# Kernel tuning notes

Hardware: AMD Instinct MI355X
Metric: run time of the kernel (lower is better)

## Reference

```python
import jax, jax.numpy as jnp
import numpy as np

N_NODES = 100000
N_EDGES = 1600000
D = 128

def setup_inputs() -> dict:
    key = jax.random.key(0)
    ks = jax.random.split(key, 6)
    x = jax.random.normal(ks[0], (N_NODES, D), dtype=jnp.float32)
    edge_src = jax.random.randint(ks[1], (N_EDGES,), 0, N_NODES, dtype=jnp.int32)
    edge_dst = jax.random.randint(ks[2], (N_EDGES,), 0, N_NODES, dtype=jnp.int32)
    # Glorot-ish scaling for 128x128 linears
    scale = 1.0 / np.sqrt(D)
    W1 = jax.random.normal(ks[3], (D, D), dtype=jnp.float32) * scale
    b1 = jnp.zeros((D,), dtype=jnp.float32)
    W2 = jax.random.normal(ks[4], (D, D), dtype=jnp.float32) * scale
    b2 = jnp.zeros((D,), dtype=jnp.float32)
    return {"x": x, "edge_src": edge_src, "edge_dst": edge_dst,
            "W1": W1, "b1": b1, "W2": W2, "b2": b2}

def reference(x, edge_src, edge_dst, W1, b1, W2, b2):
    # g.set_data('.hidden', data); g.apply(pre_mod): Linear + ReLU per node
    h = jax.nn.relu(x @ W1 + b1)                      # [N, D]
    # g.push(func=sum): each node's hidden becomes the sum of its
    # in-neighbors' hidden features (gather by src, scatter-add by dst).
    msgs = h[edge_src]                                # [E, D] irregular gather
    agg = jax.ops.segment_sum(msgs, edge_dst, num_segments=N_NODES)  # [N, D]
    # g.apply(post_mod): Linear per node; g.pop_data returns result
    out = agg @ W2 + b2                               # [N, D]
    return out
```

## Files before the change

kernel.cpp:

```cpp
#include <hip/hip_runtime.h>

#define D 128
#define NPB 256
#define NBMAX 512
#define BKCAP 8192
#define CHUNK 8192
#define OVF_CAP 8192

typedef __attribute__((ext_vector_type(8))) short short8x;
typedef __attribute__((ext_vector_type(4))) float f32x4;

__device__ inline unsigned int f2bf(float f) {
    unsigned int u = __builtin_bit_cast(unsigned int, f);
    return (u + 0x7fffu + ((u >> 16) & 1u)) >> 16;
}
__device__ inline float bflo(unsigned int v) {
    return __builtin_bit_cast(float, v << 16);
}
__device__ inline float bfhi(unsigned int v) {
    return __builtin_bit_cast(float, v & 0xffff0000u);
}
__device__ inline unsigned int pack2(float lo, float hi) {
    return f2bf(lo) | (f2bf(hi) << 16);
}

__global__ __launch_bounds__(256) void pack_w(
    const float* __restrict__ W1, const float* __restrict__ W2,
    uint4* __restrict__ pack, int* __restrict__ zero_area, int nz)
{
    if (blockIdx.x == 16) {
        for (int i = threadIdx.x; i < nz; i += 256) zero_area[i] = 0;
        return;
    }
    int e = blockIdx.x * 256 + threadIdx.x;
    const float* W = (e & 2048) ? W2 : W1;
    int f = (e >> 6) & 31, l = e & 63;
    int kt = f >> 3, nt = f & 7;
    int k0 = kt * 32 + (l >> 4) * 8;
    int col = nt * 16 + (l & 15);
    unsigned int v[8];
#pragma unroll
    for (int j = 0; j < 8; ++j) v[j] = f2bf(W[(size_t)(k0 + j) * D + col]);
    uint4 o;
    o.x = v[0] | (v[1] << 16);
    o.y = v[2] | (v[3] << 16);
    o.z = v[4] | (v[5] << 16);
    o.w = v[6] | (v[7] << 16);
    pack[e] = o;
}

__global__ __launch_bounds__(256) void build_gemm(
    const int* __restrict__ esrc, const int* __restrict__ edst,
    int* __restrict__ gfill, unsigned* __restrict__ pairs,
    int* __restrict__ ovf_cnt, int2* __restrict__ ovf_list, int E, int NB,
    int nscatter,
    const float* __restrict__ xin, const uint4* __restrict__ wpack,
    const float* __restrict__ b1, uint4* __restrict__ zout4, int n_rows)
{
    __shared__ __align__(16) char smem[65536];
    const int t = threadIdx.x;

    if (blockIdx.x < nscatter) {
        int* lcnt  = (int*)smem;
        int* lbase = lcnt + NBMAX;
        for (int b = t; b < NB; b += 256) lcnt[b] = 0;
        __syncthreads();
        int cb = blockIdx.x * CHUNK;
        int ce = min(E, cb + CHUNK);
        for (int i = cb + t; i < ce; i += 256)
            atomicAdd(&lcnt[edst[i] >> 8], 1);
        __syncthreads();
        for (int b = t; b < NB; b += 256) {
            int c = lcnt[b];
            lbase[b] = c ? atomicAdd(&gfill[b], c) : 0;
            lcnt[b] = 0;
        }
        __syncthreads();
        for (int i = cb + t; i < ce; i += 256) {
            int d = edst[i];
            int s = esrc[i];
            int b = d >> 8;
            int pos = lbase[b] + atomicAdd(&lcnt[b], 1);
            if (pos < BKCAP) {
                pairs[(size_t)b * BKCAP + pos] = ((unsigned)s << 8) | (unsigned)(d & 255);
            } else {
                int o = atomicAdd(ovf_cnt, 1);
                if (o < OVF_CAP) ovf_list[o] = make_int2(s, d);
            }
        }
        return;
    }

    uint4* ws  = (uint4*)smem;
    uint4* xs4 = ws + 2048;
    const int row0 = (blockIdx.x - nscatter) * 128;

#pragma unroll
    for (int i = 0; i < 8; ++i) ws[t + 256 * i] = wpack[t + 256 * i];

    const float4* g = (const float4*)xin;
#pragma unroll
    for (int i = 0; i < 8; ++i) {
        int c = t + 256 * i;
        int row = c >> 4, kc = c & 15;
        int grow = row0 + row;
        if (grow < n_rows) {
            float4 f0 = g[(size_t)grow * 32 + kc * 2];
            float4 f1 = g[(size_t)grow * 32 + kc * 2 + 1];
            uint4 v;
            v.x = pack2(f0.x, f0.y);
            v.y = pack2(f0.z, f0.w);
            v.z = pack2(f1.x, f1.y);
            v.w = pack2(f1.z, f1.w);
            xs4[row * 16 + (kc ^ (row & 7))] = v;
        }
    }
    __syncthreads();

    const int l = t & 63;
    const int w = t >> 6;
    const int l15 = l & 15;
    const int lk = l >> 4;
    const int arow0 = w * 32 + l15;
    const int arow1 = arow0 + 16;

    float bias1[8];
#pragma unroll
    for (int nt = 0; nt < 8; ++nt) bias1[nt] = b1[nt * 16 + l15];

    f32x4 acc1[2][8];
#pragma unroll
    for (int rt = 0; rt < 2; ++rt)
#pragma unroll
        for (int nt = 0; nt < 8; ++nt) acc1[rt][nt] = (f32x4){0.f, 0.f, 0.f, 0.f};

#pragma unroll
    for (int kt = 0; kt < 4; ++kt) {
        int kc0 = kt * 4 + lk;
        short8x a0 = *(const short8x*)&xs4[arow0 * 16 + (kc0 ^ (arow0 & 7))];
        short8x a1 = *(const short8x*)&xs4[arow1 * 16 + (kc0 ^ (arow1 & 7))];
#pragma unroll
        for (int nt = 0; nt < 8; ++nt) {
            short8x bf = *(const short8x*)&ws[(kt * 8 + nt) * 64 + l];
            acc1[0][nt] = __builtin_amdgcn_mfma_f32_16x16x32_bf16(a0, bf, acc1[0][nt], 0, 0, 0);
            acc1[1][nt] = __builtin_amdgcn_mfma_f32_16x16x32_bf16(a1, bf, acc1[1][nt], 0, 0, 0);
        }
    }

    unsigned short* hsu = (unsigned short*)xs4;
#pragma unroll
    for (int rt = 0; rt < 2; ++rt) {
#pragma unroll
        for (int nt = 0; nt < 8; ++nt) {
            int col = nt * 16 + l15;
            int ci = (col >> 3), ce2 = (col & 7);
#pragma unroll
            for (int r = 0; r < 4; ++r) {
                int rowl = w * 32 + rt * 16 + lk * 4 + r;
                float v = fmaxf(acc1[rt][nt][r] + bias1[nt], 0.f);
                hsu[(rowl * 16 + (ci ^ (rowl & 7))) * 8 + ce2] = (unsigned short)f2bf(v);
            }
        }
    }
    __syncthreads();

#pragma unroll
    for (int i = 0; i < 8; ++i) ws[t + 256 * i] = wpack[2048 + t + 256 * i];
    __syncthreads();

    f32x4 acc2[2][8];
#pragma unroll
    for (int rt = 0; rt < 2; ++rt)
#pragma unroll
        for (int nt = 0; nt < 8; ++nt) acc2[rt][nt] = (f32x4){0.f, 0.f, 0.f, 0.f};

#pragma unroll
    for (int kt = 0; kt < 4; ++kt) {
        int kc0 = kt * 4 + lk;
        short8x a0 = *(const short8x*)&xs4[arow0 * 16 + (kc0 ^ (arow0 & 7))];
        short8x a1 = *(const short8x*)&xs4[arow1 * 16 + (kc0 ^ (arow1 & 7))];
#pragma unroll
        for (int nt = 0; nt < 8; ++nt) {
            short8x bf = *(const short8x*)&ws[(kt * 8 + nt) * 64 + l];
            acc2[0][nt] = __builtin_amdgcn_mfma_f32_16x16x32_bf16(a0, bf, acc2[0][nt], 0, 0, 0);
            acc2[1][nt] = __builtin_amdgcn_mfma_f32_16x16x32_bf16(a1, bf, acc2[1][nt], 0, 0, 0);
        }
    }
    __syncthreads();

    unsigned short* zls = (unsigned short*)ws;
#pragma unroll
    for (int rt = 0; rt < 2; ++rt) {
#pragma unroll
        for (int nt = 0; nt < 8; ++nt) {
            int col = nt * 16 + l15;
#pragma unroll
            for (int r = 0; r < 4; ++r) {
                int rowl = w * 32 + rt * 16 + lk * 4 + r;
                zls[rowl * D + col] = (unsigned short)f2bf(acc2[rt][nt][r]);
            }
        }
    }
    __syncthreads();
    const uint4* zlsv = (const uint4*)zls;
#pragma unroll
    for (int i = 0; i < 8; ++i) {
        int c = t + 256 * i;
        int row = c >> 4, kc = c & 15;
        if (row0 + row < n_rows)
            zout4[(size_t)(row0 + row) * 16 + kc] = zlsv[c];
    }
}

__global__ __launch_bounds__(256) void node_sort(
    const unsigned* __restrict__ pairs, const int* __restrict__ gfill,
    int* __restrict__ srcs, int2* __restrict__ noff2, int n_nodes)
{
    __shared__ int fill[NPB];
    __shared__ int scanb[NPB];
    const int bkt = blockIdx.x;
    const int t = threadIdx.x;
    const size_t ebase = (size_t)bkt * BKCAP;
    const int ecnt = min(gfill[bkt], BKCAP);

    fill[t] = 0;
    __syncthreads();
    for (int i = t; i < ecnt; i += 256)
        atomicAdd(&fill[pairs[ebase + i] & 255], 1);
    __syncthreads();

    int c = fill[t];
    scanb[t] = c;
    __syncthreads();
    for (int s = 1; s < NPB; s <<= 1) {
        int add = (t >= s) ? scanb[t - s] : 0;
        __syncthreads();
        scanb[t] += add;
        __syncthreads();
    }
    int off = scanb[t] - c;
    int node = (bkt << 8) + t;
    if (node < n_nodes) noff2[node] = make_int2((int)ebase + off, c);
    fill[t] = off;
    __syncthreads();

    for (int i = t; i < ecnt; i += 256) {
        unsigned v = pairs[ebase + i];
        int pos = atomicAdd(&fill[v & 255], 1);
        srcs[ebase + pos] = (int)(v >> 8);
    }
}

__global__ __launch_bounds__(256) void pull_csr(
    const uint2* __restrict__ z2, const int* __restrict__ srcs,
    const int2* __restrict__ noff2, const float* __restrict__ b2,
    float* __restrict__ out, int n_nodes)
{
    int node = blockIdx.x * 8 + (threadIdx.x >> 5);
    int lane = threadIdx.x & 31;
    if (node >= n_nodes) return;
    int2 se = noff2[node];
    int i = se.x, end = se.x + se.y;

    float a0 = 0.f, a1 = 0.f, a2 = 0.f, a3 = 0.f;
    for (; i + 8 <= end; i += 8) {
        int4 sA = *(const int4*)(srcs + i);
        int4 sB = *(const int4*)(srcs + i + 4);
        uint2 v0 = z2[(size_t)sA.x * 32 + lane];
        uint2 v1 = z2[(size_t)sA.y * 32 + lane];
        uint2 v2 = z2[(size_t)sA.z * 32 + lane];
        uint2 v3 = z2[(size_t)sA.w * 32 + lane];
        uint2 v4 = z2[(size_t)sB.x * 32 + lane];
        uint2 v5 = z2[(size_t)sB.y * 32 + lane];
        uint2 v6 = z2[(size_t)sB.z * 32 + lane];
        uint2 v7 = z2[(size_t)sB.w * 32 + lane];
        a0 += bflo(v0.x) + bflo(v1.x) + bflo(v2.x) + bflo(v3.x)
            + bflo(v4.x) + bflo(v5.x) + bflo(v6.x) + bflo(v7.x);
        a1 += bfhi(v0.x) + bfhi(v1.x) + bfhi(v2.x) + bfhi(v3.x)
            + bfhi(v4.x) + bfhi(v5.x) + bfhi(v6.x) + bfhi(v7.x);
        a2 += bflo(v0.y) + bflo(v1.y) + bflo(v2.y) + bflo(v3.y)
            + bflo(v4.y) + bflo(v5.y) + bflo(v6.y) + bflo(v7.y);
        a3 += bfhi(v0.y) + bfhi(v1.y) + bfhi(v2.y) + bfhi(v3.y)
            + bfhi(v4.y) + bfhi(v5.y) + bfhi(v6.y) + bfhi(v7.y);
    }
    if (i + 4 <= end) {
        int4 s = *(const int4*)(srcs + i);
        uint2 v0 = z2[(size_t)s.x * 32 + lane];
        uint2 v1 = z2[(size_t)s.y * 32 + lane];
        uint2 v2 = z2[(size_t)s.z * 32 + lane];
        uint2 v3 = z2[(size_t)s.w * 32 + lane];
        a0 += bflo(v0.x) + bflo(v1.x) + bflo(v2.x) + bflo(v3.x);
        a1 += bfhi(v0.x) + bfhi(v1.x) + bfhi(v2.x) + bfhi(v3.x);
        a2 += bflo(v0.y) + bflo(v1.y) + bflo(v2.y) + bflo(v3.y);
        a3 += bfhi(v0.y) + bfhi(v1.y) + bfhi(v2.y) + bfhi(v3.y);
        i += 4;
    }
    for (; i < end; ++i) {
        int s = srcs[i];
        uint2 v = z2[(size_t)s * 32 + lane];
        a0 += bflo(v.x); a1 += bfhi(v.x);
        a2 += bflo(v.y); a3 += bfhi(v.y);
    }
    float4 bv = ((const float4*)b2)[lane];
    ((float4*)out)[(size_t)node * 32 + lane] =
        make_float4(a0 + bv.x, a1 + bv.y, a2 + bv.z, a3 + bv.w);
}

__global__ __launch_bounds__(32) void ovf_f32(
    const int* __restrict__ ovf_cnt, const int2* __restrict__ ovf_list,
    const uint2* __restrict__ z2, float* __restrict__ out)
{
    int n = *ovf_cnt;
    if (n > OVF_CAP) n = OVF_CAP;
    int lane = threadIdx.x;
    for (int i = blockIdx.x; i < n; i += gridDim.x) {
        int2 sd = ovf_list[i];
        uint2 v = z2[(size_t)sd.x * 32 + lane];
        unsafeAtomicAdd(&out[(size_t)sd.y * D + lane * 4 + 0], bflo(v.x));
        unsafeAtomicAdd(&out[(size_t)sd.y * D + lane * 4 + 1], bfhi(v.x));
        unsafeAtomicAdd(&out[(size_t)sd.y * D + lane * 4 + 2], bflo(v.y));
        unsafeAtomicAdd(&out[(size_t)sd.y * D + lane * 4 + 3], bfhi(v.y));
    }
}

template <bool RELU>
__global__ __launch_bounds__(256) void gemm_bias_act(
    const float* xin, const float* __restrict__ W,
    const float* __restrict__ b, float* xout, int n_rows)
{
    __shared__ float Ws[D * D];
    __shared__ float xs[32 * D];
    const int t = threadIdx.x;
    const int row0 = blockIdx.x * 32;
    const float4* Wv = (const float4*)W;
    float4* Wsv = (float4*)Ws;
#pragma unroll
    for (int i = 0; i < 16; ++i) Wsv[t + 256 * i] = Wv[t + 256 * i];
    const float4* xv = (const float4*)xin;
    float4* xsv = (float4*)xs;
#pragma unroll
    for (int i = 0; i < 4; ++i) {
        int f4 = t + 256 * i;
        int row = row0 + (f4 >> 5);
        if (row < n_rows) xsv[f4] = xv[(size_t)row0 * 32 + f4];
    }
    __syncthreads();
    const int cg = t & 31;
    const int rg = t >> 5;
    float4 bias = ((const float4*)b)[cg];
    float4 acc[4];
#pragma unroll
    for (int ri = 0; ri < 4; ++ri) acc[ri] = make_float4(0.f, 0.f, 0.f, 0.f);
#pragma unroll 4
    for (int k = 0; k < D; k += 4) {
        float4 w0 = Wsv[(k + 0) * 32 + cg];
        float4 w1 = Wsv[(k + 1) * 32 + cg];
        float4 w2 = Wsv[(k + 2) * 32 + cg];
        float4 w3 = Wsv[(k + 3) * 32 + cg];
#pragma unroll
        for (int ri = 0; ri < 4; ++ri) {
            float4 xa = xsv[(rg + 8 * ri) * 32 + (k >> 2)];
            acc[ri].x = fmaf(xa.x, w0.x, fmaf(xa.y, w1.x, fmaf(xa.z, w2.x, fmaf(xa.w, w3.x, acc[ri].x))));
            acc[ri].y = fmaf(xa.x, w0.y, fmaf(xa.y, w1.y, fmaf(xa.z, w2.y, fmaf(xa.w, w3.y, acc[ri].y))));
            acc[ri].z = fmaf(xa.x, w0.z, fmaf(xa.y, w1.z, fmaf(xa.z, w2.z, fmaf(xa.w, w3.z, acc[ri].z))));
            acc[ri].w = fmaf(xa.x, w0.w, fmaf(xa.y, w1.w, fmaf(xa.z, w2.w, fmaf(xa.w, w3.w, acc[ri].w))));
        }
    }
#pragma unroll
    for (int ri = 0; ri < 4; ++ri) {
        int row = row0 + rg + 8 * ri;
        if (row >= n_rows) continue;
        float4 o;
        o.x = acc[ri].x + bias.x; o.y = acc[ri].y + bias.y;
        o.z = acc[ri].z + bias.z; o.w = acc[ri].w + bias.w;
        if (RELU) {
            o.x = fmaxf(o.x, 0.f); o.y = fmaxf(o.y, 0.f);
            o.z = fmaxf(o.z, 0.f); o.w = fmaxf(o.w, 0.f);
        }
        ((float4*)xout)[(size_t)row * 32 + cg] = o;
    }
}

__global__ __launch_bounds__(256) void zero_kernel(float4* p, int n4)
{
    int i = blockIdx.x * 256 + threadIdx.x;
    int stride = gridDim.x * 256;
    for (; i < n4; i += stride) p[i] = make_float4(0.f, 0.f, 0.f, 0.f);
}

__global__ __launch_bounds__(256) void scatter_kernel(
    const float* __restrict__ h, const int* __restrict__ esrc,
    const int* __restrict__ edst, float* __restrict__ agg, long n_items)
{
    long idx = (long)blockIdx.x * 256 + threadIdx.x;
    long stride = (long)gridDim.x * 256;
    for (; idx < n_items; idx += stride) {
        int e = (int)(idx >> 7);
        int c = (int)(idx & 127);
        int s = esrc[e];
        int d = edst[e];
        unsafeAtomicAdd(&agg[(size_t)d * D + c], h[(size_t)s * D + c]);
    }
}

extern "C" void kernel_launch(void* const* d_in, const int* in_sizes, int n_in,
                              void* d_out, int out_size, void* d_ws, size_t ws_size,
                              hipStream_t stream)
{
    const float* x    = (const float*)d_in[0];
    const int*   esrc = (const int*)d_in[1];
    const int*   edst = (const int*)d_in[2];
    const float* W1   = (const float*)d_in[3];
    const float* b1   = (const float*)d_in[4];
    const float* W2   = (const float*)d_in[5];
    const float* b2   = (const float*)d_in[6];
    float* out = (float*)d_out;

    const int N = in_sizes[0] / D;
    const int E = in_sizes[1];
    const int NB = (N + NPB - 1) / NPB;

    char* ws = (char*)d_ws;
    size_t off_z     = 0;
    size_t off_pairs = off_z + (size_t)N * 256;
    size_t off_srcs  = off_pairs + (size_t)NBMAX * BKCAP * 4;
    size_t off_noff  = off_srcs + (size_t)NBMAX * BKCAP * 4;
    size_t off_gfill = (off_noff + (size_t)N * 8 + 255) & ~(size_t)255;
    size_t off_ovfc  = off_gfill + NBMAX * 4;
    size_t off_ovfl  = off_ovfc + 16;
    size_t off_pack  = (off_ovfl + (size_t)OVF_CAP * 8 + 255) & ~(size_t)255;
    size_t need      = off_pack + 65536;

    const int gchunk = (E + CHUNK - 1) / CHUNK;
    const int nblk128 = (N + 127) / 128;

    if (ws_size >= need && N <= NBMAX * NPB) {
        uint4*    z4    = (uint4*)(ws + off_z);
        unsigned* pairs = (unsigned*)(ws + off_pairs);
        int*      srcs  = (int*)(ws + off_srcs);
        int2*     noff2 = (int2*)(ws + off_noff);
        int*      gfill = (int*)(ws + off_gfill);
        int*      ovfc  = (int*)(ws + off_ovfc);
        int2*     ovfl  = (int2*)(ws + off_ovfl);
        uint4*    pack  = (uint4*)(ws + off_pack);

        pack_w<<<17, 256, 0, stream>>>(W1, W2, pack, gfill, NBMAX + 4);

        build_gemm<<<gchunk + nblk128, 256, 0, stream>>>(
            esrc, edst, gfill, pairs, ovfc, ovfl, E, NB, gchunk,
            x, pack, b1, z4, N);

        node_sort<<<NB, 256, 0, stream>>>(pairs, gfill, srcs, noff2, N);

        pull_csr<<<(N + 7) / 8, 256, 0, stream>>>(
            (const uint2*)z4, srcs, noff2, b2, out, N);

        ovf_f32<<<8, 32, 0, stream>>>(ovfc, ovfl, (const uint2*)z4, out);
    } else {
        float* h = (float*)ws;
        const int nb32 = (N + 31) / 32;
        gemm_bias_act<true><<<nb32, 256, 0, stream>>>(x, W1, b1, h, N);
        zero_kernel<<<2048, 256, 0, stream>>>((float4*)out, N * D / 4);
        scatter_kernel<<<8192, 256, 0, stream>>>(h, esrc, edst, out, (long)E * D);
        gemm_bias_act<false><<<nb32, 256, 0, stream>>>(out, W2, b2, out, N);
    }
}
```

Measured before the change: 121.2 us.

## Split first GEMM across scatter and sort kernels to overlap with edge bucketing

Moves the node GEMM tile code into a shared device function and splits its row blocks: 3/5 run alongside the edge-bucketing scatter blocks and the rest run alongside the per-bucket node sort blocks. Sort blocks were only NB (~391) blocks with little work each, so adding GEMM blocks to that launch is meant to fill otherwise idle CUs and balance the two kernels. The node_sort kernel now declares a 64KB shared buffer, which may lower occupancy for the sort blocks.

```diff
diff --git a/kernel.cpp b/kernel.cpp
--- a/kernel.cpp
+++ b/kernel.cpp
@@ -49,51 +49,14 @@
     pack[e] = o;
 }
 
-__global__ __launch_bounds__(256) void build_gemm(
-    const int* __restrict__ esrc, const int* __restrict__ edst,
-    int* __restrict__ gfill, unsigned* __restrict__ pairs,
-    int* __restrict__ ovf_cnt, int2* __restrict__ ovf_list, int E, int NB,
-    int nscatter,
+__device__ __forceinline__ void gemm_tile(
+    char* smem, int row0,
     const float* __restrict__ xin, const uint4* __restrict__ wpack,
     const float* __restrict__ b1, uint4* __restrict__ zout4, int n_rows)
 {
-    __shared__ __align__(16) char smem[65536];
     const int t = threadIdx.x;
-
-    if (blockIdx.x < nscatter) {
-        int* lcnt  = (int*)smem;
-        int* lbase = lcnt + NBMAX;
-        for (int b = t; b < NB; b += 256) lcnt[b] = 0;
-        __syncthreads();
-        int cb = blockIdx.x * CHUNK;
-        int ce = min(E, cb + CHUNK);
-        for (int i = cb + t; i < ce; i += 256)
-            atomicAdd(&lcnt[edst[i] >> 8], 1);
-        __syncthreads();
-        for (int b = t; b < NB; b += 256) {
-            int c = lcnt[b];
-            lbase[b] = c ? atomicAdd(&gfill[b], c) : 0;
-            lcnt[b] = 0;
-        }
-        __syncthreads();
-        for (int i = cb + t; i < ce; i += 256) {
-            int d = edst[i];
-            int s = esrc[i];
-            int b = d >> 8;
-            int pos = lbase[b] + atomicAdd(&lcnt[b], 1);
-            if (pos < BKCAP) {
-                pairs[(size_t)b * BKCAP + pos] = ((unsigned)s << 8) | (unsigned)(d & 255);
-            } else {
-                int o = atomicAdd(ovf_cnt, 1);
-                if (o < OVF_CAP) ovf_list[o] = make_int2(s, d);
-            }
-        }
-        return;
-    }
-
     uint4* ws  = (uint4*)smem;
     uint4* xs4 = ws + 2048;
-    const int row0 = (blockIdx.x - nscatter) * 128;
 
 #pragma unroll
     for (int i = 0; i < 8; ++i) ws[t + 256 * i] = wpack[t + 256 * i];
@@ -212,43 +175,96 @@
     }
 }
 
-__global__ __launch_bounds__(256) void node_sort(
+__global__ __launch_bounds__(256) void scatter_gemm(
+    const int* __restrict__ esrc, const int* __restrict__ edst,
+    int* __restrict__ gfill, unsigned* __restrict__ pairs,
+    int* __restrict__ ovf_cnt, int2* __restrict__ ovf_list, int E, int NB,
+    int nscatter,
+    const float* __restrict__ xin, const uint4* __restrict__ wpack,
+    const float* __restrict__ b1, uint4* __restrict__ zout4, int n_rows)
+{
+    __shared__ __align__(16) char smem[65536];
+    const int t = threadIdx.x;
+
+    if (blockIdx.x < nscatter) {
+        int* lcnt  = (int*)smem;
+        int* lbase = lcnt + NBMAX;
+        for (int b = t; b < NB; b += 256) lcnt[b] = 0;
+        __syncthreads();
+        int cb = blockIdx.x * CHUNK;
+        int ce = min(E, cb + CHUNK);
+        for (int i = cb + t; i < ce; i += 256)
+            atomicAdd(&lcnt[edst[i] >> 8], 1);
+        __syncthreads();
+        for (int b = t; b < NB; b += 256) {
+            int c = lcnt[b];
+            lbase[b] = c ? atomicAdd(&gfill[b], c) : 0;
+            lcnt[b] = 0;
+        }
+        __syncthreads();
+        for (int i = cb + t; i < ce; i += 256) {
+            int d = edst[i];
+            int s = esrc[i];
+            int b = d >> 8;
+            int pos = lbase[b] + atomicAdd(&lcnt[b], 1);
+            if (pos < BKCAP) {
+                pairs[(size_t)b * BKCAP + pos] = ((unsigned)s << 8) | (unsigned)(d & 255);
+            } else {
+                int o = atomicAdd(ovf_cnt, 1);
+                if (o < OVF_CAP) ovf_list[o] = make_int2(s, d);
+            }
+        }
+        return;
+    }
+    gemm_tile(smem, (blockIdx.x - nscatter) * 128, xin, wpack, b1, zout4, n_rows);
+}
+
+__global__ __launch_bounds__(256) void sort_gemm(
     const unsigned* __restrict__ pairs, const int* __restrict__ gfill,
-    int* __restrict__ srcs, int2* __restrict__ noff2, int n_nodes)
-{
-    __shared__ int fill[NPB];
-    __shared__ int scanb[NPB];
-    const int bkt = blockIdx.x;
+    int* __restrict__ srcs, int2* __restrict__ noff2, int n_nodes, int nsort,
+    const float* __restrict__ xin, const uint4* __restrict__ wpack,
+    const float* __restrict__ b1, uint4* __restrict__ zout4, int n_rows,
+    int gemm_blk0)
+{
+    __shared__ __align__(16) char smem[65536];
     const int t = threadIdx.x;
-    const size_t ebase = (size_t)bkt * BKCAP;
-    const int ecnt = min(gfill[bkt], BKCAP);
-
-    fill[t] = 0;
-    __syncthreads();
-    for (int i = t; i < ecnt; i += 256)
-        atomicAdd(&fill[pairs[ebase + i] & 255], 1);
-    __syncthreads();
-
-    int c = fill[t];
-    scanb[t] = c;
-    __syncthreads();
-    for (int s = 1; s < NPB; s <<= 1) {
-        int add = (t >= s) ? scanb[t - s] : 0;
-        __syncthreads();
-        scanb[t] += add;
-        __syncthreads();
-    }
-    int off = scanb[t] - c;
-    int node = (bkt << 8) + t;
-    if (node < n_nodes) noff2[node] = make_int2((int)ebase + off, c);
-    fill[t] = off;
-    __syncthreads();
-
-    for (int i = t; i < ecnt; i += 256) {
-        unsigned v = pairs[ebase + i];
-        int pos = atomicAdd(&fill[v & 255], 1);
-        srcs[ebase + pos] = (int)(v >> 8);
-    }
+
+    if (blockIdx.x < (unsigned)nsort) {
+        int* fill  = (int*)smem;
+        int* scanb = fill + NPB;
+        const int bkt = blockIdx.x;
+        const size_t ebase = (size_t)bkt * BKCAP;
+        const int ecnt = min(gfill[bkt], BKCAP);
+
+        fill[t] = 0;
+        __syncthreads();
+        for (int i = t; i < ecnt; i += 256)
+            atomicAdd(&fill[pairs[ebase + i] & 255], 1);
+        __syncthreads();
+
+        int c = fill[t];
+        scanb[t] = c;
+        __syncthreads();
+        for (int s = 1; s < NPB; s <<= 1) {
+            int add = (t >= s) ? scanb[t - s] : 0;
+            __syncthreads();
+            scanb[t] += add;
+            __syncthreads();
+        }
+        int off = scanb[t] - c;
+        int node = (bkt << 8) + t;
+        if (node < n_nodes) noff2[node] = make_int2((int)ebase + off, c);
+        fill[t] = off;
+        __syncthreads();
+
+        for (int i = t; i < ecnt; i += 256) {
+            unsigned v = pairs[ebase + i];
+            int pos = atomicAdd(&fill[v & 255], 1);
+            srcs[ebase + pos] = (int)(v >> 8);
+        }
+        return;
+    }
+    gemm_tile(smem, (blockIdx.x - nsort + gemm_blk0) * 128, xin, wpack, b1, zout4, n_rows);
 }
 
 __global__ __launch_bounds__(256) void pull_csr(
@@ -431,8 +447,10 @@
     size_t off_pack  = (off_ovfl + (size_t)OVF_CAP * 8 + 255) & ~(size_t)255;
     size_t need      = off_pack + 65536;
 
-    const int gchunk = (E + CHUNK - 1) / CHUNK;
+    const int gchunk  = (E + CHUNK - 1) / CHUNK;
     const int nblk128 = (N + 127) / 128;
+    const int gemmA   = (nblk128 * 3) / 5;
+    const int gemmB   = nblk128 - gemmA;
 
     if (ws_size >= need && N <= NBMAX * NPB) {
         uint4*    z4    = (uint4*)(ws + off_z);
@@ -446,11 +464,13 @@
 
         pack_w<<<17, 256, 0, stream>>>(W1, W2, pack, gfill, NBMAX + 4);
 
-        build_gemm<<<gchunk + nblk128, 256, 0, stream>>>(
+        scatter_gemm<<<gchunk + gemmA, 256, 0, stream>>>(
             esrc, edst, gfill, pairs, ovfc, ovfl, E, NB, gchunk,
             x, pack, b1, z4, N);
 
-        node_sort<<<NB, 256, 0, stream>>>(pairs, gfill, srcs, noff2, N);
+        sort_gemm<<<NB + gemmB, 256, 0, stream>>>(
+            pairs, gfill, srcs, noff2, N, NB,
+            x, pack, b1, z4, N, gemmA);
 
         pull_csr<<<(N + 7) / 8, 256, 0, stream>>>(
             (const uint2*)z4, srcs, noff2, b2, out, N);
```

Result: slower. 124.3 us (+2.6%).

## Fuse per-bucket node sort with CSR pull aggregation into one kernel

Applied to the files above, without the earlier changes.

Merges the bucket counting sort and the gather-sum pull into a single 1024-thread kernel per 256-node bucket. The sorted source list stays in LDS instead of being written to global srcs/noff2 and read back, and one kernel launch is removed. In exchange there are only about 391 blocks of 1024 threads, each using about 34KB of LDS, so occupancy and parallelism for the latency-bound gather drop compared with the previous 12.5k-block pull kernel.

```diff
diff --git a/kernel.cpp b/kernel.cpp
--- a/kernel.cpp
+++ b/kernel.cpp
@@ -212,98 +212,108 @@
     }
 }
 
-__global__ __launch_bounds__(256) void node_sort(
+__global__ __launch_bounds__(1024) void sort_pull(
     const unsigned* __restrict__ pairs, const int* __restrict__ gfill,
-    int* __restrict__ srcs, int2* __restrict__ noff2, int n_nodes)
-{
+    const uint2* __restrict__ z2, const float* __restrict__ b2,
+    float* __restrict__ out, int n_nodes)
+{
+    __shared__ int srcl[BKCAP];
+    __shared__ int off[NPB + 1];
     __shared__ int fill[NPB];
     __shared__ int scanb[NPB];
+
     const int bkt = blockIdx.x;
     const int t = threadIdx.x;
     const size_t ebase = (size_t)bkt * BKCAP;
     const int ecnt = min(gfill[bkt], BKCAP);
 
-    fill[t] = 0;
-    __syncthreads();
-    for (int i = t; i < ecnt; i += 256)
-        atomicAdd(&fill[pairs[ebase + i] & 255], 1);
-    __syncthreads();
-
-    int c = fill[t];
-    scanb[t] = c;
+    if (t < NPB) fill[t] = 0;
+    __syncthreads();
+
+    unsigned pv0, pv1, pv2, pv3, pv4, pv5, pv6, pv7;
+#define LOADP(K, PV) { int i = t + (K) * 1024; \
+        PV = (i < ecnt) ? pairs[ebase + i] : 0xFFFFFFFFu; \
+        if (i < ecnt) atomicAdd(&fill[PV & 255], 1); }
+    LOADP(0, pv0) LOADP(1, pv1) LOADP(2, pv2) LOADP(3, pv3)
+    LOADP(4, pv4) LOADP(5, pv5) LOADP(6, pv6) LOADP(7, pv7)
+#undef LOADP
+    __syncthreads();
+
+    if (t < NPB) scanb[t] = fill[t];
     __syncthreads();
     for (int s = 1; s < NPB; s <<= 1) {
-        int add = (t >= s) ? scanb[t - s] : 0;
+        int add = 0;
+        if (t < NPB && t >= s) add = scanb[t - s];
         __syncthreads();
-        scanb[t] += add;
+        if (t < NPB) scanb[t] += add;
         __syncthreads();
     }
-    int off = scanb[t] - c;
-    int node = (bkt << 8) + t;
-    if (node < n_nodes) noff2[node] = make_int2((int)ebase + off, c);
-    fill[t] = off;
-    __syncthreads();
-
-    for (int i = t; i < ecnt; i += 256) {
-        unsigned v = pairs[ebase + i];
-        int pos = atomicAdd(&fill[v & 255], 1);
-        srcs[ebase + pos] = (int)(v >> 8);
-    }
-}
-
-__global__ __launch_bounds__(256) void pull_csr(
-    const uint2* __restrict__ z2, const int* __restrict__ srcs,
-    const int2* __restrict__ noff2, const float* __restrict__ b2,
-    float* __restrict__ out, int n_nodes)
-{
-    int node = blockIdx.x * 8 + (threadIdx.x >> 5);
-    int lane = threadIdx.x & 31;
-    if (node >= n_nodes) return;
-    int2 se = noff2[node];
-    int i = se.x, end = se.x + se.y;
-
-    float a0 = 0.f, a1 = 0.f, a2 = 0.f, a3 = 0.f;
-    for (; i + 8 <= end; i += 8) {
-        int4 sA = *(const int4*)(srcs + i);
-        int4 sB = *(const int4*)(srcs + i + 4);
-        uint2 v0 = z2[(size_t)sA.x * 32 + lane];
-        uint2 v1 = z2[(size_t)sA.y * 32 + lane];
-        uint2 v2 = z2[(size_t)sA.z * 32 + lane];
-        uint2 v3 = z2[(size_t)sA.w * 32 + lane];
-        uint2 v4 = z2[(size_t)sB.x * 32 + lane];
-        uint2 v5 = z2[(size_t)sB.y * 32 + lane];
-        uint2 v6 = z2[(size_t)sB.z * 32 + lane];
-        uint2 v7 = z2[(size_t)sB.w * 32 + lane];
-        a0 += bflo(v0.x) + bflo(v1.x) + bflo(v2.x) + bflo(v3.x)
-            + bflo(v4.x) + bflo(v5.x) + bflo(v6.x) + bflo(v7.x);
-        a1 += bfhi(v0.x) + bfhi(v1.x) + bfhi(v2.x) + bfhi(v3.x)
-            + bfhi(v4.x) + bfhi(v5.x) + bfhi(v6.x) + bfhi(v7.x);
-        a2 += bflo(v0.y) + bflo(v1.y) + bflo(v2.y) + bflo(v3.y)
-            + bflo(v4.y) + bflo(v5.y) + bflo(v6.y) + bflo(v7.y);
-        a3 += bfhi(v0.y) + bfhi(v1.y) + bfhi(v2.y) + bfhi(v3.y)
-            + bfhi(v4.y) + bfhi(v5.y) + bfhi(v6.y) + bfhi(v7.y);
-    }
-    if (i + 4 <= end) {
-        int4 s = *(const int4*)(srcs + i);
-        uint2 v0 = z2[(size_t)s.x * 32 + lane];
-        uint2 v1 = z2[(size_t)s.y * 32 + lane];
-        uint2 v2 = z2[(size_t)s.z * 32 + lane];
-        uint2 v3 = z2[(size_t)s.w * 32 + lane];
-        a0 += bflo(v0.x) + bflo(v1.x) + bflo(v2.x) + bflo(v3.x);
-        a1 += bfhi(v0.x) + bfhi(v1.x) + bfhi(v2.x) + bfhi(v3.x);
-        a2 += bflo(v0.y) + bflo(v1.y) + bflo(v2.y) + bflo(v3.y);
-        a3 += bfhi(v0.y) + bfhi(v1.y) + bfhi(v2.y) + bfhi(v3.y);
-        i += 4;
-    }
-    for (; i < end; ++i) {
-        int s = srcs[i];
-        uint2 v = z2[(size_t)s * 32 + lane];
-        a0 += bflo(v.x); a1 += bfhi(v.x);
-        a2 += bflo(v.y); a3 += bfhi(v.y);
-    }
+    if (t < NPB) {
+        int c = fill[t];
+        off[t] = scanb[t] - c;
+        fill[t] = scanb[t] - c;
+    }
+    if (t == 0) off[NPB] = ecnt;
+    __syncthreads();
+
+#define SCATP(K, PV) { int i = t + (K) * 1024; \
+        if (i < ecnt) { int pos = atomicAdd(&fill[PV & 255], 1); \
+            srcl[pos] = (int)(PV >> 8); } }
+    SCATP(0, pv0) SCATP(1, pv1) SCATP(2, pv2) SCATP(3, pv3)
+    SCATP(4, pv4) SCATP(5, pv5) SCATP(6, pv6) SCATP(7, pv7)
+#undef SCATP
+    __syncthreads();
+
+    const int grp = t >> 5;
+    const int lane = t & 31;
     float4 bv = ((const float4*)b2)[lane];
-    ((float4*)out)[(size_t)node * 32 + lane] =
-        make_float4(a0 + bv.x, a1 + bv.y, a2 + bv.z, a3 + bv.w);
+
+    for (int ln = grp; ln < NPB; ln += 32) {
+        int node = (bkt << 8) + ln;
+        if (node >= n_nodes) break;
+        int i = off[ln], end = off[ln + 1];
+
+        float a0 = 0.f, a1 = 0.f, a2 = 0.f, a3 = 0.f;
+        for (; i + 8 <= end; i += 8) {
+            int s0 = srcl[i],     s1 = srcl[i + 1], s2 = srcl[i + 2], s3 = srcl[i + 3];
+            int s4 = srcl[i + 4], s5 = srcl[i + 5], s6 = srcl[i + 6], s7 = srcl[i + 7];
+            uint2 v0 = z2[(size_t)s0 * 32 + lane];
+            uint2 v1 = z2[(size_t)s1 * 32 + lane];
+            uint2 v2 = z2[(size_t)s2 * 32 + lane];
+            uint2 v3 = z2[(size_t)s3 * 32 + lane];
+            uint2 v4 = z2[(size_t)s4 * 32 + lane];
+            uint2 v5 = z2[(size_t)s5 * 32 + lane];
+            uint2 v6 = z2[(size_t)s6 * 32 + lane];
+            uint2 v7 = z2[(size_t)s7 * 32 + lane];
+            a0 += bflo(v0.x) + bflo(v1.x) + bflo(v2.x) + bflo(v3.x)
+                + bflo(v4.x) + bflo(v5.x) + bflo(v6.x) + bflo(v7.x);
+            a1 += bfhi(v0.x) + bfhi(v1.x) + bfhi(v2.x) + bfhi(v3.x)
+                + bfhi(v4.x) + bfhi(v5.x) + bfhi(v6.x) + bfhi(v7.x);
+            a2 += bflo(v0.y) + bflo(v1.y) + bflo(v2.y) + bflo(v3.y)
+                + bflo(v4.y) + bflo(v5.y) + bflo(v6.y) + bflo(v7.y);
+            a3 += bfhi(v0.y) + bfhi(v1.y) + bfhi(v2.y) + bfhi(v3.y)
+                + bfhi(v4.y) + bfhi(v5.y) + bfhi(v6.y) + bfhi(v7.y);
+        }
+        if (i + 4 <= end) {
+            int s0 = srcl[i], s1 = srcl[i + 1], s2 = srcl[i + 2], s3 = srcl[i + 3];
+            uint2 v0 = z2[(size_t)s0 * 32 + lane];
+            uint2 v1 = z2[(size_t)s1 * 32 + lane];
+            uint2 v2 = z2[(size_t)s2 * 32 + lane];
+            uint2 v3 = z2[(size_t)s3 * 32 + lane];
+            a0 += bflo(v0.x) + bflo(v1.x) + bflo(v2.x) + bflo(v3.x);
+            a1 += bfhi(v0.x) + bfhi(v1.x) + bfhi(v2.x) + bfhi(v3.x);
+            a2 += bflo(v0.y) + bflo(v1.y) + bflo(v2.y) + bflo(v3.y);
+            a3 += bfhi(v0.y) + bfhi(v1.y) + bfhi(v2.y) + bfhi(v3.y);
+            i += 4;
+        }
+        for (; i < end; ++i) {
+            uint2 v = z2[(size_t)srcl[i] * 32 + lane];
+            a0 += bflo(v.x); a1 += bfhi(v.x);
+            a2 += bflo(v.y); a3 += bfhi(v.y);
+        }
+        ((float4*)out)[(size_t)node * 32 + lane] =
+            make_float4(a0 + bv.x, a1 + bv.y, a2 + bv.z, a3 + bv.w);
+    }
 }
 
 __global__ __launch_bounds__(32) void ovf_f32(
@@ -423,22 +433,18 @@
     char* ws = (char*)d_ws;
     size_t off_z     = 0;
     size_t off_pairs = off_z + (size_t)N * 256;
-    size_t off_srcs  = off_pairs + (size_t)NBMAX * BKCAP * 4;
-    size_t off_noff  = off_srcs + (size_t)NBMAX * BKCAP * 4;
-    size_t off_gfill = (off_noff + (size_t)N * 8 + 255) & ~(size_t)255;
+    size_t off_gfill = (off_pairs + (size_t)NBMAX * BKCAP * 4 + 255) & ~(size_t)255;
     size_t off_ovfc  = off_gfill + NBMAX * 4;
     size_t off_ovfl  = off_ovfc + 16;
     size_t off_pack  = (off_ovfl + (size_t)OVF_CAP * 8 + 255) & ~(size_t)255;
     size_t need      = off_pack + 65536;
 
-    const int gchunk = (E + CHUNK - 1) / CHUNK;
+    const int gchunk  = (E + CHUNK - 1) / CHUNK;
     const int nblk128 = (N + 127) / 128;
 
     if (ws_size >= need && N <= NBMAX * NPB) {
         uint4*    z4    = (uint4*)(ws + off_z);
         unsigned* pairs = (unsigned*)(ws + off_pairs);
-        int*      srcs  = (int*)(ws + off_srcs);
-        int2*     noff2 = (int2*)(ws + off_noff);
         int*      gfill = (int*)(ws + off_gfill);
         int*      ovfc  = (int*)(ws + off_ovfc);
         int2*     ovfl  = (int2*)(ws + off_ovfl);
@@ -450,10 +456,8 @@
             esrc, edst, gfill, pairs, ovfc, ovfl, E, NB, gchunk,
             x, pack, b1, z4, N);
 
-        node_sort<<<NB, 256, 0, stream>>>(pairs, gfill, srcs, noff2, N);
-
-        pull_csr<<<(N + 7) / 8, 256, 0, stream>>>(
-            (const uint2*)z4, srcs, noff2, b2, out, N);
+        sort_pull<<<NB, 1024, 0, stream>>>(
+            pairs, gfill, (const uint2*)z4, b2, out, N);
 
         ovf_f32<<<8, 32, 0, stream>>>(ovfc, ovfl, (const uint2*)z4, out);
     } else {
```

New measurement: 113.0 us. 6.7% less time.
